# Optimization experiments

Measured on AMD Instinct MI355X. Metric: run time of the kernel, lower is better.

The kernel has to match this reference:

```python
import jax, jax.numpy as jnp
import numpy as np

B, KLEN, QLEN = 16, 4096, 1
D_MODEL, HEADS, KERNELS = 1024, 8, 10
DIM = D_MODEL // HEADS  # 128
SCALE = 0.02


def setup_inputs() -> dict:
    key = jax.random.key(0)
    ks = jax.random.split(key, 12)
    return {
        "query": jax.random.normal(ks[0], (B, QLEN, D_MODEL), jnp.float32),
        "key_in": jax.random.normal(ks[1], (B, KLEN, D_MODEL), jnp.float32),
        "value": jax.random.normal(ks[2], (B, KLEN, D_MODEL), jnp.float32),
        "prev_align": jax.random.uniform(ks[3], (B, HEADS, KLEN), jnp.float32),
        # learned params
        "conv_w": jax.random.normal(ks[4], (KERNELS, HEADS, 3), jnp.float32) * SCALE,   # OIH, k=3
        "conv_b": jnp.zeros((KERNELS,), jnp.float32),
        "w_u": jax.random.normal(ks[5], (KERNELS, DIM), jnp.float32) * SCALE,
        "w_q": jax.random.normal(ks[6], (D_MODEL, HEADS * DIM), jnp.float32) * SCALE,
        "w_v": jax.random.normal(ks[7], (D_MODEL, HEADS * DIM), jnp.float32) * SCALE,
        "bias": jax.random.uniform(ks[8], (DIM,), jnp.float32, minval=-0.1, maxval=0.1),
        "score_w": jax.random.normal(ks[9], (DIM,), jnp.float32) * SCALE,
        "score_b": jnp.zeros((), jnp.float32),
    }


def reference(query, key_in, value, prev_align, conv_w, conv_b, w_u, w_q, w_v, bias, score_w, score_b):
    b, k_len = key_in.shape[0], key_in.shape[1]
    # location features: conv1d over k_len with heads as channels -> [B, KERNELS, k_len]
    loc = jax.lax.conv_general_dilated(
        prev_align, conv_w, window_strides=(1,), padding=[(1, 1)],
        dimension_numbers=("NCH", "OIH", "NCH")) + conv_b[None, :, None]
    loc_energy = jnp.tanh(jnp.einsum("bck,cd->bkd", loc, w_u))  # [B, k_len, DIM]
    # projections split into heads
    q = jnp.einsum("bqf,fe->bqe", query, w_q).reshape(b, QLEN, HEADS, DIM).transpose(0, 2, 1, 3)   # [B,H,1,DIM]
    k = jnp.einsum("bkf,fe->bke", key_in, w_v).reshape(b, k_len, HEADS, DIM).transpose(0, 2, 1, 3)  # [B,H,K,DIM]
    v = value.reshape(b, k_len, HEADS, DIM).transpose(0, 2, 1, 3)                                   # [B,H,K,DIM]
    # additive energy (q_len==1 broadcasts over keys)
    e = jnp.tanh(k + q + loc_energy[:, None] + bias)            # [B,H,K,DIM]
    score = jnp.einsum("bhkd,d->bhk", e, score_w) + score_b    # [B,H,K]
    align = jax.nn.softmax(score, axis=-1)
    context = jnp.einsum("bhk,bhkd->bhd", align, v).reshape(b * HEADS, DIM)
    return context, align
```

## Files before the change

kernel.cpp:

```cpp
#include <hip/hip_runtime.h>
#include <hip/hip_bf16.h>
#include <cstdint>

typedef __attribute__((ext_vector_type(8))) short bf16x8;
typedef __attribute__((ext_vector_type(4))) float f32x4;
typedef __attribute__((ext_vector_type(8))) unsigned short u16x8;
typedef __attribute__((ext_vector_type(4))) unsigned int u32x4;

__device__ __forceinline__ unsigned short f2bf(float f) {
    unsigned int u = __float_as_uint(f);
    unsigned int r = (u + 0x7fffu + ((u >> 16) & 1u)) >> 16;
    return (unsigned short)r;
}

__device__ __forceinline__ float tanh_fast(float x) {
    return 1.0f - 2.0f / (__expf(2.0f * x) + 1.0f);
}

#define GLDS(SRC, DST) __builtin_amdgcn_global_load_lds(                         \
        (const __attribute__((address_space(1))) void*)(SRC),                    \
        (__attribute__((address_space(3))) void*)(DST), 16, 0, 0)

__global__ __launch_bounds__(256) void prep_kernel(
        const float* __restrict__ wv, unsigned short* __restrict__ wvT,
        const float* __restrict__ query, const float* __restrict__ w_q,
        float* __restrict__ ws_q,
        const float* __restrict__ pa, const float* __restrict__ conv_w,
        const float* __restrict__ conv_b, const float* __restrict__ w_u,
        float* __restrict__ le, float* __restrict__ ctx_out,
        float* __restrict__ rowsum) {
    __shared__ __align__(16) char smem[16640];
    const int bid = blockIdx.x;
    const int t = threadIdx.x;

    if (bid < 256) {
        float (*tile)[129] = reinterpret_cast<float(*)[129]>(smem);
        const int h = bid >> 5, kt = bid & 31;
        for (int i = t; i < 1024; i += 256) {
            const int fl = i >> 5;
            const int e4 = (i & 31) * 4;
            const float4 v = *reinterpret_cast<const float4*>(
                wv + (size_t)(kt * 32 + fl) * 1024 + h * 128 + e4);
            tile[fl][e4 + 0] = v.x; tile[fl][e4 + 1] = v.y;
            tile[fl][e4 + 2] = v.z; tile[fl][e4 + 3] = v.w;
        }
        __syncthreads();
#pragma unroll
        for (int cc2 = 0; cc2 < 2; ++cc2) {
            const int c = cc2 * 256 + t;
            const int cb = c >> 6, kg = (c >> 4) & 3, ccl = c & 15;
            const int e_local = cb * 16 + ccl;
            u16x8 u;
#pragma unroll
            for (int jj = 0; jj < 8; ++jj) u[jj] = f2bf(tile[kg * 8 + jj][e_local]);
            *reinterpret_cast<u16x8*>(wvT + (((size_t)h * 32 + kt) * 512 + c) * 8) = u;
        }
    } else if (bid < 384) {
        float* qs = reinterpret_cast<float*>(smem);
        const int bh = bid - 256;
        const int b = bh >> 3, h = bh & 7;
        for (int i = t; i < 1024; i += 256) qs[i] = query[(size_t)b * 1024 + i];
        __syncthreads();
        if (t < 128) {
            float acc = 0.f;
            const float* wcol = w_q + h * 128 + t;
            for (int f = 0; f < 1024; ++f) acc = fmaf(qs[f], wcol[(size_t)f * 1024], acc);
            ws_q[(size_t)bh * 128 + t] = acc;
        }
    } else if (bid < 896) {
        float* pas = reinterpret_cast<float*>(smem);
        float* wu_s = pas + 1056;
        float* cw = wu_s + 1280;
        float* cb = cw + 240;
        const int idx = bid - 384;
        const int b = idx >> 5, k0 = (idx & 31) * 128;
        for (int i = t; i < 8 * 130; i += 256) {
            const int hh = i / 130, kk = i % 130;
            const int gk = k0 + kk - 1;
            pas[hh * 132 + kk] = (gk >= 0 && gk < 4096)
                ? pa[((size_t)(b * 8 + hh)) * 4096 + gk] : 0.f;
        }
        for (int i = t; i < 1280; i += 256) wu_s[i] = w_u[i];
        if (t < 240) cw[t] = conv_w[t];
        if (t < 10) cb[t] = conv_b[t];
        __syncthreads();
        const int k = t >> 1;
        const int d0 = (t & 1) * 64;
        float lc[10];
#pragma unroll
        for (int c = 0; c < 10; ++c) {
            float acc = cb[c];
#pragma unroll
            for (int hh = 0; hh < 8; ++hh) {
                acc += pas[hh * 132 + k] * cw[(c * 8 + hh) * 3 + 0]
                     + pas[hh * 132 + k + 1] * cw[(c * 8 + hh) * 3 + 1]
                     + pas[hh * 132 + k + 2] * cw[(c * 8 + hh) * 3 + 2];
            }
            lc[c] = acc;
        }
        float* dst = le + ((size_t)(b * 4096) + k0 + k) * 128 + d0;
#pragma unroll
        for (int dd = 0; dd < 64; dd += 4) {
            float4 o;
#pragma unroll
            for (int jj = 0; jj < 4; ++jj) {
                float s = 0.f;
#pragma unroll
                for (int c = 0; c < 10; ++c) s += lc[c] * wu_s[c * 128 + d0 + dd + jj];
                ((float*)&o)[jj] = tanh_fast(s);
            }
            *reinterpret_cast<float4*>(dst + dd) = o;
        }
    } else {
        float4 z = {0.f, 0.f, 0.f, 0.f};
        for (int i = t; i < 4096; i += 256)
            *reinterpret_cast<float4*>(ctx_out + (size_t)i * 4) = z;
        if (t < 128) rowsum[t] = 0.f;
    }
}

#define NT 32
__global__ __launch_bounds__(512) void gemm_score_kernel(
        const float* __restrict__ key_in, const unsigned short* __restrict__ wvT_tiled,
        const float* __restrict__ le,
        const float* __restrict__ ws_q, const float* __restrict__ bias,
        const float* __restrict__ score_w, const float* __restrict__ score_b,
        float* __restrict__ align_out, float* __restrict__ rowsum) {
    __shared__ __align__(16) unsigned short As[3][4096];
    __shared__ __align__(16) unsigned short Bs[3][8192];
    __shared__ float qb_sm[256], sw_sm[128];
    __shared__ float partial[128][4];

    const int t = threadIdx.x;
    const int lane = t & 63, wid = t >> 6;
    const int wm = wid >> 2;
    const int wn = wid & 3;

    const int fid = blockIdx.x;
    const int x = fid & 7, j = fid >> 3;
    const int bm = x * 64 + (j >> 2);
    const int hp = j & 3;
    const int b = bm >> 5;
    const int kk0 = (bm & 31) << 7;

    if (t < 256) {
        const int hh = t >> 7, d = t & 127;
        qb_sm[t] = ws_q[(size_t)(b * 8 + hp * 2 + hh) * 128 + d] + bias[d];
        if (t < 128) sw_sm[t] = score_w[t];
    }

    const int r_ = t >> 2, ks = t & 3;
    const float* aRow = key_in + ((size_t)(b * 4096 + kk0) + r_) * 1024 + ks * 8;
    const int cW = (t >> 6) * 64 + ks * 16 + (r_ & 15);
    const int dst0 = (cW ^ (ks | ((ks & 1) << 2))) * 8;

    const int kgR = lane >> 4;
    const int laneSwz = lane ^ (kgR | ((kgR & 1) << 2));

    const unsigned short* bT = wvT_tiled
        + (size_t)(hp * 2 + (t >> 8)) * 131072 + (t & 255) * 8;
    const int dstB = (t >> 8) * 4096 + (t & 255) * 8;

    float4 st0, st1;

#define LOADA(KT) {                                                               \
        const float* p_ = aRow + (KT) * 32;                                       \
        st0 = *reinterpret_cast<const float4*>(p_);                               \
        st1 = *reinterpret_cast<const float4*>(p_ + 4); }

#define WRITEA(BUF) {                                                             \
        __hip_bfloat162 h0_ = __float22bfloat162_rn({st0.x, st0.y});              \
        __hip_bfloat162 h1_ = __float22bfloat162_rn({st0.z, st0.w});              \
        __hip_bfloat162 h2_ = __float22bfloat162_rn({st1.x, st1.y});              \
        __hip_bfloat162 h3_ = __float22bfloat162_rn({st1.z, st1.w});              \
        u32x4 u_;                                                                 \
        u_[0] = *reinterpret_cast<unsigned int*>(&h0_);                           \
        u_[1] = *reinterpret_cast<unsigned int*>(&h1_);                           \
        u_[2] = *reinterpret_cast<unsigned int*>(&h2_);                           \
        u_[3] = *reinterpret_cast<unsigned int*>(&h3_);                           \
        *reinterpret_cast<u32x4*>(&As[BUF][dst0]) = u_; }

#define STAGE_B(BUF, KT) {                                                        \
        GLDS(bT + (size_t)(KT) * 4096, &Bs[BUF][dstB]);                           \
        GLDS(bT + (size_t)(KT) * 4096 + 2048, &Bs[BUF][dstB + 2048]); }

    f32x4 acc[4][4] = {};

    LOADA(0);
    STAGE_B(0, 0);
    WRITEA(0);
    LOADA(1);

    for (int kt = 0; kt < NT; ++kt) {
        const int cur = kt % 3;
        const int nxt = (kt + 1) % 3;
        STAGE_B(nxt, (kt + 1) & (NT - 1));
        WRITEA(nxt);
        LOADA((kt + 2) & (NT - 1));
        asm volatile("s_waitcnt lgkmcnt(0)\n\t"
                     "s_barrier" ::: "memory");

        bf16x8 af[4], bg[4];
#pragma unroll
        for (int mf = 0; mf < 4; ++mf)
            af[mf] = *reinterpret_cast<const bf16x8*>(
                &As[cur][((wm * 4 + mf) * 64 + laneSwz) * 8]);
#pragma unroll
        for (int nf = 0; nf < 4; ++nf)
            bg[nf] = *reinterpret_cast<const bf16x8*>(
                &Bs[cur][(wn >> 1) * 4096 + ((wn & 1) * 4 + nf) * 512 + lane * 8]);
        __builtin_amdgcn_s_setprio(1);
#pragma unroll
        for (int mf = 0; mf < 4; ++mf)
#pragma unroll
            for (int nf = 0; nf < 4; ++nf)
                acc[mf][nf] = __builtin_amdgcn_mfma_f32_16x16x32_bf16(
                    af[mf], bg[nf], acc[mf][nf], 0, 0, 0);
        __builtin_amdgcn_s_setprio(0);
    }

    const float K2 = 2.8853900817779268f;
    const float LOG2E = 1.4426950408889634f;
    const float sb = score_b[0];
    const int g = lane >> 4;
    const int l15 = lane & 15;
    float kqb[4], swv[4];
#pragma unroll
    for (int nf = 0; nf < 4; ++nf) {
        const int d128 = (wn & 1) * 64 + nf * 16 + l15;
        kqb[nf] = qb_sm[(wn >> 1) * 128 + d128] * K2;
        swv[nf] = sw_sm[d128];
    }
    const float* leB = le + ((size_t)(b * 4096 + kk0) + wm * 64 + g * 4) * 128
                       + (wn & 1) * 64 + l15;

#pragma unroll
    for (int mf = 0; mf < 4; ++mf) {
        float lv[16];
#pragma unroll
        for (int jj = 0; jj < 4; ++jj)
#pragma unroll
            for (int nf = 0; nf < 4; ++nf)
                lv[jj * 4 + nf] = leB[(size_t)(mf * 16 + jj) * 128 + nf * 16];
#pragma unroll
        for (int jj = 0; jj < 4; ++jj) {
            const int row_l = wm * 64 + mf * 16 + g * 4 + jj;
            float sum = 0.f;
#pragma unroll
            for (int nf = 0; nf < 4; ++nf) {
                const float m = fmaf(K2, lv[jj * 4 + nf], kqb[nf]);
                const float tt = fmaf(K2, acc[mf][nf][jj], m);
                const float y = __builtin_amdgcn_exp2f(tt);
                const float r = fmaf(-2.0f, __builtin_amdgcn_rcpf(y + 1.0f), 1.0f);
                sum = fmaf(r, swv[nf], sum);
            }
            sum += __shfl_xor(sum, 1);
            sum += __shfl_xor(sum, 2);
            sum += __shfl_xor(sum, 4);
            sum += __shfl_xor(sum, 8);
            if (l15 == 0) partial[row_l][wn] = sum;
        }
    }
    __syncthreads();
    if (t < 256) {
        const int r = t >> 1, hh = t & 1;
        const float sc = partial[r][hh * 2] + partial[r][hh * 2 + 1] + sb;
        const float e = __builtin_amdgcn_exp2f(sc * LOG2E);
        align_out[(size_t)(b * 8 + hp * 2 + hh) * 4096 + kk0 + r] = e;
        float s = e;
        s += __shfl_xor(s, 2);
        s += __shfl_xor(s, 4);
        s += __shfl_xor(s, 8);
        s += __shfl_xor(s, 16);
        s += __shfl_xor(s, 32);
        if ((lane >> 1) == 0)
            atomicAdd(&rowsum[b * 8 + hp * 2 + hh], s);
    }
}

__global__ __launch_bounds__(256) void ctx_partial_kernel(
        const float* __restrict__ value, float* __restrict__ align_o,
        const float* __restrict__ rowsum, float* __restrict__ ctx_out) {
    const int s = blockIdx.x;
    const int bh = blockIdx.y;
    const int b = bh >> 3, h = bh & 7;
    const int t = threadIdx.x;
    const int d4 = (t & 31) * 4;
    const int kg = t >> 5;
    const float inv = 1.0f / rowsum[bh];
    float* arow = align_o + (size_t)bh * 4096 + s * 128;
    const float* vbase = value + ((size_t)(b * 4096 + s * 128)) * 1024 + h * 128 + d4;
    float4 acc = {0.f, 0.f, 0.f, 0.f};
    for (int i = 0; i < 16; ++i) {
        const int kk = i * 8 + kg;
        const float a = arow[kk];
        const float4 v = *reinterpret_cast<const float4*>(vbase + (size_t)kk * 1024);
        acc.x += a * v.x; acc.y += a * v.y; acc.z += a * v.z; acc.w += a * v.w;
    }
    __shared__ float sm2[8][128];
    *reinterpret_cast<float4*>(&sm2[kg][d4]) = acc;
    __syncthreads();
    if (t < 128) {
        float s0 = 0.f;
#pragma unroll
        for (int gg = 0; gg < 8; ++gg) s0 += sm2[gg][t];
        atomicAdd(&ctx_out[(size_t)bh * 128 + t], s0 * inv);
        arow[t] *= inv;
    }
}

extern "C" void kernel_launch(void* const* d_in, const int* in_sizes, int n_in,
                              void* d_out, int out_size, void* d_ws, size_t ws_size,
                              hipStream_t stream) {
    const float* query   = (const float*)d_in[0];
    const float* key_in  = (const float*)d_in[1];
    const float* value   = (const float*)d_in[2];
    const float* pa      = (const float*)d_in[3];
    const float* conv_w  = (const float*)d_in[4];
    const float* conv_b  = (const float*)d_in[5];
    const float* w_u     = (const float*)d_in[6];
    const float* w_q     = (const float*)d_in[7];
    const float* w_v     = (const float*)d_in[8];
    const float* bias    = (const float*)d_in[9];
    const float* score_w = (const float*)d_in[10];
    const float* score_b = (const float*)d_in[11];

    float* out = (float*)d_out;
    float* ctx_out = out;
    float* align_out = out + 16384;

    char* ws = (char*)d_ws;
    const size_t OFF_Q    = 0;
    const size_t OFF_RS   = 65536;
    const size_t OFF_WVT  = 66048;
    const size_t OFF_LE   = OFF_WVT + 2097152;

    float* ws_q            = (float*)(ws + OFF_Q);
    float* ws_rs           = (float*)(ws + OFF_RS);
    unsigned short* ws_wvT = (unsigned short*)(ws + OFF_WVT);
    float* ws_le           = (float*)(ws + OFF_LE);

    hipLaunchKernelGGL(prep_kernel, dim3(897), dim3(256), 0, stream,
                       w_v, ws_wvT, query, w_q, ws_q,
                       pa, conv_w, conv_b, w_u, ws_le, ctx_out, ws_rs);
    hipLaunchKernelGGL(gemm_score_kernel, dim3(2048), dim3(512), 0, stream,
                       key_in, ws_wvT, ws_le, ws_q, bias, score_w, score_b,
                       align_out, ws_rs);
    hipLaunchKernelGGL(ctx_partial_kernel, dim3(32, 128), dim3(256), 0, stream,
                       value, align_out, ws_rs, ctx_out);
}
```

Baseline: 285.7 us.

## Fuse context accumulation into score GEMM kernel, normalize in finalize pass

Moves the align-weighted value reduction into the score kernel, using the unnormalized exponentials kept in shared memory so value is read right after the scores are made. A small finalize kernel then divides both align and the context by the row sums. This removes the separate pass that reread align and value and saves a kernel launch. In exchange it adds a barrier and a scalar strided value load loop to the GEMM kernel, and more atomics per block.

```diff
diff --git a/kernel.cpp b/kernel.cpp
--- a/kernel.cpp
+++ b/kernel.cpp
@@ -122,14 +122,16 @@
 #define NT 32
 __global__ __launch_bounds__(512) void gemm_score_kernel(
         const float* __restrict__ key_in, const unsigned short* __restrict__ wvT_tiled,
-        const float* __restrict__ le,
+        const float* __restrict__ le, const float* __restrict__ value,
         const float* __restrict__ ws_q, const float* __restrict__ bias,
         const float* __restrict__ score_w, const float* __restrict__ score_b,
-        float* __restrict__ align_out, float* __restrict__ rowsum) {
+        float* __restrict__ align_out, float* __restrict__ rowsum,
+        float* __restrict__ ctx_out) {
     __shared__ __align__(16) unsigned short As[3][4096];
     __shared__ __align__(16) unsigned short Bs[3][8192];
     __shared__ float qb_sm[256], sw_sm[128];
     __shared__ float partial[128][4];
+    __shared__ float e_sm[256];
 
     const int t = threadIdx.x;
     const int lane = t & 63, wid = t >> 6;
@@ -267,6 +269,7 @@
         const float sc = partial[r][hh * 2] + partial[r][hh * 2 + 1] + sb;
         const float e = __builtin_amdgcn_exp2f(sc * LOG2E);
         align_out[(size_t)(b * 8 + hp * 2 + hh) * 4096 + kk0 + r] = e;
+        e_sm[hh * 128 + r] = e;
         float s = e;
         s += __shfl_xor(s, 2);
         s += __shfl_xor(s, 4);
@@ -276,36 +279,44 @@
         if ((lane >> 1) == 0)
             atomicAdd(&rowsum[b * 8 + hp * 2 + hh], s);
     }
-}
-
-__global__ __launch_bounds__(256) void ctx_partial_kernel(
-        const float* __restrict__ value, float* __restrict__ align_o,
-        const float* __restrict__ rowsum, float* __restrict__ ctx_out) {
-    const int s = blockIdx.x;
-    const int bh = blockIdx.y;
-    const int b = bh >> 3, h = bh & 7;
+    __syncthreads();
+
+    {
+        const int col = t & 255;
+        const int p = t >> 8;
+        const float* vcol = value + ((size_t)(b * 4096 + kk0 + p)) * 1024
+                            + hp * 256 + col;
+        const float* es = &e_sm[(col >> 7) * 128 + p];
+        float acc2 = 0.f;
+#pragma unroll 8
+        for (int i = 0; i < 64; ++i)
+            acc2 = fmaf(es[2 * i], vcol[(size_t)(2 * i) * 1024], acc2);
+        float* comb = &partial[0][0];
+        comb[t] = acc2;
+        __syncthreads();
+        if (t < 256) {
+            const float tot = comb[t] + comb[t + 256];
+            atomicAdd(&ctx_out[(size_t)(b * 8 + hp * 2 + (col >> 7)) * 128
+                               + (col & 127)], tot);
+        }
+    }
+}
+
+__global__ __launch_bounds__(256) void finalize_kernel(
+        float* __restrict__ align_o, float* __restrict__ ctx_out,
+        const float* __restrict__ rowsum) {
+    const int bid = blockIdx.x;
     const int t = threadIdx.x;
-    const int d4 = (t & 31) * 4;
-    const int kg = t >> 5;
-    const float inv = 1.0f / rowsum[bh];
-    float* arow = align_o + (size_t)bh * 4096 + s * 128;
-    const float* vbase = value + ((size_t)(b * 4096 + s * 128)) * 1024 + h * 128 + d4;
-    float4 acc = {0.f, 0.f, 0.f, 0.f};
-    for (int i = 0; i < 16; ++i) {
-        const int kk = i * 8 + kg;
-        const float a = arow[kk];
-        const float4 v = *reinterpret_cast<const float4*>(vbase + (size_t)kk * 1024);
-        acc.x += a * v.x; acc.y += a * v.y; acc.z += a * v.z; acc.w += a * v.w;
-    }
-    __shared__ float sm2[8][128];
-    *reinterpret_cast<float4*>(&sm2[kg][d4]) = acc;
-    __syncthreads();
-    if (t < 128) {
-        float s0 = 0.f;
-#pragma unroll
-        for (int gg = 0; gg < 8; ++gg) s0 += sm2[gg][t];
-        atomicAdd(&ctx_out[(size_t)bh * 128 + t], s0 * inv);
-        arow[t] *= inv;
+    if (bid < 512) {
+        const int bh = bid >> 2;
+        const float inv = 1.0f / rowsum[bh];
+        float4* p = reinterpret_cast<float4*>(align_o + (size_t)bid * 1024);
+        float4 v = p[t];
+        v.x *= inv; v.y *= inv; v.z *= inv; v.w *= inv;
+        p[t] = v;
+    } else {
+        const int i = (bid - 512) * 256 + t;
+        ctx_out[i] *= 1.0f / rowsum[i >> 7];
     }
 }
 
@@ -344,8 +355,8 @@
                        w_v, ws_wvT, query, w_q, ws_q,
                        pa, conv_w, conv_b, w_u, ws_le, ctx_out, ws_rs);
     hipLaunchKernelGGL(gemm_score_kernel, dim3(2048), dim3(512), 0, stream,
-                       key_in, ws_wvT, ws_le, ws_q, bias, score_w, score_b,
-                       align_out, ws_rs);
-    hipLaunchKernelGGL(ctx_partial_kernel, dim3(32, 128), dim3(256), 0, stream,
-                       value, align_out, ws_rs, ctx_out);
-}
+                       key_in, ws_wvT, ws_le, value, ws_q, bias, score_w, score_b,
+                       align_out, ws_rs, ctx_out);
+    hipLaunchKernelGGL(finalize_kernel, dim3(576), dim3(256), 0, stream,
+                       align_out, ctx_out, ws_rs);
+}
```

Result: faster. 272.7 us (median of 2 runs) (-4.6%).
